# Optimization experiments

Measured on AMD Instinct MI355X. Metric: run time of the kernel, lower is better.

## Reference

```python
import jax, jax.numpy as jnp
import numpy as np

T = 512      # block_size
E = 64       # n_embed
H = 2 * E    # ffn hidden = out = 2*n_embed


def setup_inputs() -> dict:
    key = jax.random.key(0)
    k1, k2, k3, k4, k5 = jax.random.split(key, 5)
    s = 0.02
    return {
        "b": 2,
        "pos_table": jax.random.normal(k1, (T, E), dtype=jnp.float32) * s,
        "W1": jax.random.normal(k2, (E, H), dtype=jnp.float32) * s,
        "b1": jnp.zeros((H,), dtype=jnp.float32),
        "W2": jax.random.normal(k3, (H, H), dtype=jnp.float32) * s,
        "b2": jnp.zeros((H,), dtype=jnp.float32),
    }


def reference(b, pos_table, W1, b1, W2, b2):
    n = pos_table.shape[0]
    # distance_triangle: tril(i - j), values in [0, n-1]
    dist = jnp.tril(jnp.arange(n)[:, None] - jnp.arange(n)[None, :])  # [T,T] int
    emb = pos_table[dist]                                             # [T,T,E] gather
    emb = jnp.broadcast_to(emb[None], (b,) + emb.shape)               # repeat(b,1,1,1)
    h = jax.nn.gelu(emb @ W1 + b1, approximate=False)                 # [b,T,T,2E]
    return h @ W2 + b2                                                # [b,T,T,2E]
```

## Files before the change

### kernel.cpp

```cpp
#include <hip/hip_runtime.h>
#include <math.h>

#define TT 512
#define EE 64
#define HH 128

__global__ __launch_bounds__(512) void rows_kernel(
        const float* __restrict__ pos,
        const float* __restrict__ W1,
        const float* __restrict__ b1,
        const float* __restrict__ W2,
        const float* __restrict__ b2,
        float* __restrict__ rows) {
    const int d = blockIdx.x;
    const int t = threadIdx.x;
    const int c = t & (HH - 1);
    const int s = t >> 7;

    __shared__ float p[EE];
    __shared__ float part[4][HH];
    __shared__ float h[HH];

    if (t < EE) p[t] = pos[d * EE + t];
    __syncthreads();

    float acc = (s == 0) ? b1[c] : 0.0f;
    const int e0 = s * (EE / 4);
#pragma unroll
    for (int e = 0; e < EE / 4; ++e)
        acc += p[e0 + e] * W1[(e0 + e) * HH + c];
    part[s][c] = acc;
    __syncthreads();

    float hv = part[0][c] + part[1][c] + part[2][c] + part[3][c];
    hv = 0.5f * hv * (1.0f + erff(hv * 0.7071067811865475f));
    if (s == 0) h[c] = hv;
    __syncthreads();

    float acc2 = (s == 0) ? b2[c] : 0.0f;
    const int k0 = s * (HH / 4);
#pragma unroll
    for (int k = 0; k < HH / 4; ++k)
        acc2 += h[k0 + k] * W2[(k0 + k) * HH + c];
    part[s][c] = acc2;
    __syncthreads();

    if (s == 0)
        rows[d * HH + c] = part[0][c] + part[1][c] + part[2][c] + part[3][c];
}

__global__ void scatter_kernel(const float4* __restrict__ rows4,
                               float4* __restrict__ out4) {
    const long idx = (long)blockIdx.x * blockDim.x + threadIdx.x;
    const int  q = (int)(idx & 31);
    const long r = idx >> 5;
    const int  j = (int)(r & (TT - 1));
    const int  i = (int)((r >> 9) & (TT - 1));
    const int  d = (i >= j) ? (i - j) : 0;
    out4[idx] = rows4[d * (HH / 4) + q];
}

extern "C" void kernel_launch(void* const* d_in, const int* in_sizes, int n_in,
                              void* d_out, int out_size, void* d_ws, size_t ws_size,
                              hipStream_t stream) {
    const float* pos = (const float*)d_in[1];
    const float* W1  = (const float*)d_in[2];
    const float* b1  = (const float*)d_in[3];
    const float* W2  = (const float*)d_in[4];
    const float* b2  = (const float*)d_in[5];
    float* out  = (float*)d_out;
    float* rows = (float*)d_ws;

    rows_kernel<<<TT, 512, 0, stream>>>(pos, W1, b1, W2, b2, rows);

    const bool sizes_in_bytes = (in_sizes[1] == TT * EE * 4);
    const long total_floats   = sizes_in_bytes ? (long)out_size / 4
                                               : (long)out_size;
    const long total4 = total_floats / 4;
    const int  block  = 256;
    const long grid   = (total4 + block - 1) / block;
    scatter_kernel<<<dim3((unsigned)grid), dim3(block), 0, stream>>>(
        (const float4*)rows, (float4*)out);
}
```

Baseline: 263.7 us.

## Fuse row computation with diagonal-wise scatter into a single kernel

Merges the row MLP kernel and the scatter kernel into one launch. Each lower-triangle block computes its distance row and writes it straight along its diagonal, and extra blocks broadcast row 0 over the strict upper triangle using triangular index inversion. This removes the workspace round-trip and the per-element gather read, so the work becomes a pure write stream. The costs are uneven work per block (diagonal lengths vary), a sqrt-based index decode for upper-triangle elements, and every upper block redoing the small MLP for d=0.

```diff
diff --git a/kernel.cpp b/kernel.cpp
--- a/kernel.cpp
+++ b/kernel.cpp
@@ -4,60 +4,96 @@
 #define TT 512
 #define EE 64
 #define HH 128
+#define NBLK_U 1536
+#define UCNT (TT * (TT - 1) / 2)
 
-__global__ __launch_bounds__(512) void rows_kernel(
+__device__ __forceinline__ int tri_off(int i) {
+    return (TT - 1) * i - (i * (i - 1)) / 2;
+}
+
+__global__ __launch_bounds__(256) void fused_kernel(
         const float* __restrict__ pos,
         const float* __restrict__ W1,
         const float* __restrict__ b1,
         const float* __restrict__ W2,
         const float* __restrict__ b2,
-        float* __restrict__ rows) {
-    const int d = blockIdx.x;
+        float4* __restrict__ out4,
+        int bN) {
     const int t = threadIdx.x;
     const int c = t & (HH - 1);
     const int s = t >> 7;
 
+    const bool is_lower = (blockIdx.x < TT);
+    const int d = is_lower ? blockIdx.x : 0;
+
     __shared__ float p[EE];
-    __shared__ float part[4][HH];
-    __shared__ float h[HH];
+    __shared__ float part[2][HH];
+    __shared__ float hs[HH];
+    __shared__ float row_s[HH];
 
     if (t < EE) p[t] = pos[d * EE + t];
     __syncthreads();
 
     float acc = (s == 0) ? b1[c] : 0.0f;
-    const int e0 = s * (EE / 4);
-#pragma unroll
-    for (int e = 0; e < EE / 4; ++e)
-        acc += p[e0 + e] * W1[(e0 + e) * HH + c];
+    {
+        const int e0 = s * (EE / 2);
+#pragma unroll 8
+        for (int e = 0; e < EE / 2; ++e)
+            acc += p[e0 + e] * W1[(e0 + e) * HH + c];
+    }
     part[s][c] = acc;
     __syncthreads();
 
-    float hv = part[0][c] + part[1][c] + part[2][c] + part[3][c];
-    hv = 0.5f * hv * (1.0f + erff(hv * 0.7071067811865475f));
-    if (s == 0) h[c] = hv;
+    if (s == 0) {
+        float hv = part[0][c] + part[1][c];
+        hs[c] = 0.5f * hv * (1.0f + erff(hv * 0.7071067811865475f));
+    }
     __syncthreads();
 
     float acc2 = (s == 0) ? b2[c] : 0.0f;
-    const int k0 = s * (HH / 4);
-#pragma unroll
-    for (int k = 0; k < HH / 4; ++k)
-        acc2 += h[k0 + k] * W2[(k0 + k) * HH + c];
+    {
+        const int k0 = s * (HH / 2);
+#pragma unroll 8
+        for (int k = 0; k < HH / 2; ++k)
+            acc2 += hs[k0 + k] * W2[(k0 + k) * HH + c];
+    }
     part[s][c] = acc2;
     __syncthreads();
+    if (s == 0) row_s[c] = part[0][c] + part[1][c];
+    __syncthreads();
 
-    if (s == 0)
-        rows[d * HH + c] = part[0][c] + part[1][c] + part[2][c] + part[3][c];
-}
+    const int q  = t & 31;
+    const int rl = t >> 5;
+    const float4 v = reinterpret_cast<const float4*>(row_s)[q];
 
-__global__ void scatter_kernel(const float4* __restrict__ rows4,
-                               float4* __restrict__ out4) {
-    const long idx = (long)blockIdx.x * blockDim.x + threadIdx.x;
-    const int  q = (int)(idx & 31);
-    const long r = idx >> 5;
-    const int  j = (int)(r & (TT - 1));
-    const int  i = (int)((r >> 9) & (TT - 1));
-    const int  d = (i >= j) ? (i - j) : 0;
-    out4[idx] = rows4[d * (HH / 4) + q];
+    if (is_lower) {
+        const int n = TT - d;
+        for (int bb = 0; bb < bN; ++bb) {
+            const long base_b = (long)bb * TT * TT;
+            for (int j = rl; j < n; j += 8) {
+                const long r = base_b + (long)(j + d) * TT + j;
+                out4[r * (HH / 4) + q] = v;
+            }
+        }
+    } else {
+        const int  e   = blockIdx.x - TT;
+        const long NUP = (long)bN * UCNT;
+        for (long g = (long)e * 8 + rl; g < NUP; g += (long)NBLK_U * 8) {
+            int  bb = 0;
+            long uu = g;
+            while (uu >= UCNT) { uu -= UCNT; ++bb; }
+            const int ui = (int)uu;
+            const float fa = (float)(1023 * 1023 - 8 * ui);
+            int i = (int)((1023.0f - sqrtf(fa)) * 0.5f);
+            if (i < 0) i = 0;
+            if (i > TT - 2) i = TT - 2;
+            while (tri_off(i + 1) <= ui) ++i;
+            while (i > 0 && tri_off(i) > ui) --i;
+            const int j = i + 1 + (ui - tri_off(i));
+            const long r = (long)bb * TT * TT + (long)i * TT + j;
+            out4[r * (HH / 4) + q] = v;
+        }
+    }
 }
 
 extern "C" void kernel_launch(void* const* d_in, const int* in_sizes, int n_in,
@@ -68,17 +104,13 @@
     const float* b1  = (const float*)d_in[3];
     const float* W2  = (const float*)d_in[4];
     const float* b2  = (const float*)d_in[5];
-    float* out  = (float*)d_out;
-    float* rows = (float*)d_ws;
-
-    rows_kernel<<<TT, 512, 0, stream>>>(pos, W1, b1, W2, b2, rows);
+    float4* out4 = (float4*)d_out;
 
     const bool sizes_in_bytes = (in_sizes[1] == TT * EE * 4);
     const long total_floats   = sizes_in_bytes ? (long)out_size / 4
                                                : (long)out_size;
-    const long total4 = total_floats / 4;
-    const int  block  = 256;
-    const long grid   = (total4 + block - 1) / block;
-    scatter_kernel<<<dim3((unsigned)grid), dim3(block), 0, stream>>>(
-        (const float4*)rows, (float4*)out);
+    int bN = (int)(total_floats / ((long)TT * TT * HH));
+    if (bN < 1) bN = 1;
+
+    fused_kernel<<<TT + NBLK_U, 256, 0, stream>>>(pos, W1, b1, W2, b2, out4, bN);
 }
```

New measurement: 277.4 us. 5.2% more time.
